# Optimization experiments

Measured on AMD Instinct MI355X. Metric: run time of the kernel, lower is better.

## Reference

```python
import jax, jax.numpy as jnp
import numpy as np

B, N, E = 16, 10000, 160000
C_IN, C_SP, C_OUT = 32, 16, 32


def _glorot(key, shape):
    s = float(np.sqrt(6.0 / (shape[0] + shape[1])))
    return jax.random.uniform(key, shape, jnp.float32, -s, s)


def setup_inputs() -> dict:
    key = jax.random.key(0)
    ks = jax.random.split(key, 12)
    X = jax.random.normal(ks[0], (B, N, C_IN), jnp.float32)
    edge_index1 = jax.random.randint(ks[1], (2, E), 0, N)
    edge_weight1 = jax.random.uniform(ks[2], (E,), jnp.float32)
    res_n_id1 = jnp.arange(N)
    edge_index2 = jax.random.randint(ks[3], (2, E), 0, N)
    edge_weight2 = jax.random.uniform(ks[4], (E,), jnp.float32)
    res_n_id2 = jnp.arange(N)
    # conv1 params (in=C_IN, out=C_SP, edge_channels=1, concat=True)
    amp_w1 = _glorot(ks[5], (1, C_IN))            # [edge_ch, in]
    gate_w1 = _glorot(ks[6], (2 * C_IN + 1, 1))   # Linear(2*in+edge_ch, 1)
    gate_b1 = jnp.zeros((1,), jnp.float32)
    w1 = _glorot(ks[7], (2 * C_IN, C_SP))         # concat weight
    b1 = jnp.zeros((C_SP,), jnp.float32)
    # conv2 params (in=C_SP, out=C_OUT)
    amp_w2 = _glorot(ks[8], (1, C_SP))
    gate_w2 = _glorot(ks[9], (2 * C_SP + 1, 1))
    gate_b2 = jnp.zeros((1,), jnp.float32)
    w2 = _glorot(ks[10], (2 * C_SP, C_OUT))
    b2 = jnp.zeros((C_OUT,), jnp.float32)
    return dict(X=X, edge_index1=edge_index1, edge_weight1=edge_weight1, res_n_id1=res_n_id1,
                edge_index2=edge_index2, edge_weight2=edge_weight2, res_n_id2=res_n_id2,
                amp_w1=amp_w1, gate_w1=gate_w1, gate_b1=gate_b1, w1=w1, b1=b1,
                amp_w2=amp_w2, gate_w2=gate_w2, gate_b2=gate_b2, w2=w2, b2=b2)


def _sagela(x_src, x_dst, edge_index, edge_weight, amp_w, gate_w, gate_b, w, b):
    # x_src: [B, N_src, C], x_dst: [B, N_dst, C]
    src, dst = edge_index[0], edge_index[1]
    n_dst = x_dst.shape[1]
    C = x_src.shape[-1]
    x_j = x_src[:, src]                       # [B, E, C] gathered source feats
    x_i = x_dst[:, dst]                       # [B, E, C] gathered target feats
    e = edge_weight[:, None]                  # [E, 1] edge features
    # gate_linear(cat[x_i, x_j, e]) split into three matmuls (same math)
    wg_i, wg_j, wg_e = gate_w[:C], gate_w[C:2 * C], gate_w[2 * C:]
    lamb = jax.nn.sigmoid(x_i @ wg_i + x_j @ wg_j + (e @ wg_e)[None] + gate_b)  # [B, E, 1]
    amp = e @ amp_w                           # [E, C] edge amplification
    msg = amp[None, :, :] * x_j * lamb        # [B, E, C]
    # mean aggregation over incoming edges (scatter-add / count)
    aggr = jnp.zeros((x_src.shape[0], n_dst, C), msg.dtype).at[:, dst].add(msg)
    cnt = jnp.zeros((n_dst,), msg.dtype).at[dst].add(1.0)
    aggr = aggr / jnp.maximum(cnt, 1.0)[None, :, None]
    out = jnp.concatenate([x_dst, aggr], axis=-1) @ w + b  # [B, N_dst, out]
    return out


def reference(X, edge_index1, edge_weight1, res_n_id1, edge_index2, edge_weight2, res_n_id2,
              amp_w1, gate_w1, gate_b1, w1, b1, amp_w2, gate_w2, gate_b2, w2, b2):
    h = _sagela(X, X[:, res_n_id1], edge_index1, edge_weight1, amp_w1, gate_w1, gate_b1, w1, b1)
    h = jax.nn.leaky_relu(h, 0.01)
    out = _sagela(h, h[:, res_n_id2], edge_index2, edge_weight2, amp_w2, gate_w2, gate_b2, w2, b2)
    return out
```

## Files before the change

kernel.cpp:

```cpp
#include <hip/hip_runtime.h>
#include <math.h>

#define B 16
#define N 10000
#define E 160000
#define CAP 96

__device__ __forceinline__ ushort f2bf(float v) {
    uint u = __float_as_uint(v);
    u = (u + 0x7fffu + ((u >> 16) & 1u)) >> 16;
    return (ushort)u;
}
__device__ __forceinline__ float bf2f(ushort u) { return __uint_as_float(((uint)u) << 16); }
__device__ __forceinline__ float bf2f_lo(uint u) { return __uint_as_float(u << 16); }
__device__ __forceinline__ float bf2f_hi(uint u) { return __uint_as_float(u & 0xffff0000u); }
__device__ __forceinline__ float dec_ew(uint u) {
    return ((float)(u >> 14) + 0.5f) * (1.0f / 262144.0f);
}

__global__ __launch_bounds__(256)
void prep_bucket_kernel(const float* __restrict__ X,
                        const float* __restrict__ gate_w1,
                        const int* __restrict__ ei1, const float* __restrict__ ew1,
                        const int* __restrict__ ei2, const float* __restrict__ ew2,
                        ushort* __restrict__ xt,
                        float* __restrict__ gi, float* __restrict__ gj,
                        int* __restrict__ bcount1, uint* __restrict__ bucket1,
                        int* __restrict__ bcount2, uint* __restrict__ bucket2) {
    int gtid = blockIdx.x * 256 + threadIdx.x;
    int gs = gridDim.x * 256;

    for (int t = gtid; t < 2 * E; t += gs) {
        if (t < E) {
            int d = ei1[E + t];
            int pos = atomicAdd(&bcount1[d], 1);
            if (pos < CAP) {
                uint q = (uint)(ew1[t] * 262144.0f);
                if (q > 262143u) q = 262143u;
                bucket1[d * CAP + pos] = (q << 14) | (uint)ei1[t];
            }
        } else {
            int e = t - E;
            int d = ei2[E + e];
            int pos = atomicAdd(&bcount2[d], 1);
            if (pos < CAP) {
                uint q = (uint)(ew2[e] * 262144.0f);
                if (q > 262143u) q = 262143u;
                bucket2[d * CAP + pos] = (q << 14) | (uint)ei2[e];
            }
        }
    }
    for (int t = gtid; t < N * B * 32; t += gs) {
        int c = t & 31;
        int r = t >> 5;
        int b = r & 15;
        int n = r >> 4;
        float v = X[((size_t)b * N + n) * 32 + c];
        xt[t] = f2bf(v);
        float pi = v * gate_w1[c];
        float pj = v * gate_w1[32 + c];
        #pragma unroll
        for (int off = 16; off; off >>= 1) {
            pi += __shfl_xor(pi, off, 32);
            pj += __shfl_xor(pj, off, 32);
        }
        if (c == 0) { gi[r] = pi; gj[r] = pj; }
    }
}

__global__ __launch_bounds__(256, 8)
void agg_dense1_kernel(const float* __restrict__ X,
                       const uint2* __restrict__ xt2,
                       const float* __restrict__ gi,
                       const float* __restrict__ gj,
                       const int* __restrict__ bcount,
                       const uint* __restrict__ bucket,
                       const float* __restrict__ gate_w,
                       const float* __restrict__ gate_b,
                       const float* __restrict__ amp_w,
                       const float* __restrict__ w1,
                       const float* __restrict__ b1,
                       const float* __restrict__ gate_w2,
                       ushort* __restrict__ htb,
                       float* __restrict__ gi2, float* __restrict__ gj2) {
    __shared__ uint  s_eb[CAP];
    __shared__ float s_coef[CAP * 16];
    __shared__ float s_gi[16];
    __shared__ __align__(16) float s_x[16][36];
    __shared__ __align__(16) float s_feat[16][36];
    __shared__ __align__(16) float s_wmT[16 * 68];

    int n = blockIdx.x;
    int tid = threadIdx.x;

    int cnt = bcount[n];
    int deg = cnt < CAP ? cnt : CAP;
    if (tid < deg) s_eb[tid] = bucket[n * CAP + tid];
    for (int i = tid; i < 1024; i += 256) s_wmT[(i & 15) * 68 + (i >> 4)] = w1[i];
    for (int i = tid; i < 512; i += 256) {
        int b = i >> 5, c = i & 31;
        s_x[b][c] = X[((size_t)b * N + n) * 32 + c];
    }
    if (tid < 16) s_gi[tid] = gi[n * 16 + tid] + gate_b[0];
    __syncthreads();

    float wge = gate_w[64];
    for (int p = tid; p < deg * 16; p += 256) {
        int k = p >> 4, b = p & 15;
        uint pr = s_eb[k];
        float w = dec_ew(pr);
        float z = s_gi[b] + gj[(pr & 0x3FFFu) * 16 + b] + w * wge;
        s_coef[p] = w / (1.0f + __expf(-z));
    }
    __syncthreads();

    int wv = tid >> 6, l = tid & 63;
    int h = l >> 5;
    int b = 4 * wv + ((l & 31) >> 3);
    int c4 = l & 7;
    uint boff = (uint)b * 8 + c4;
    float a0 = 0.f, a1 = 0.f, a2 = 0.f, a3 = 0.f;
    int k = 0;
    for (; k + 7 < deg; k += 8) {
        uint p0 = s_eb[k + h],     p1 = s_eb[k + 2 + h];
        uint p2 = s_eb[k + 4 + h], p3 = s_eb[k + 6 + h];
        float c0 = s_coef[((k + h) << 4) | b],     c1 = s_coef[((k + 2 + h) << 4) | b];
        float c2 = s_coef[((k + 4 + h) << 4) | b], c3 = s_coef[((k + 6 + h) << 4) | b];
        uint2 u0 = xt2[(p0 & 0x3FFFu) * 128 + boff];
        uint2 u1 = xt2[(p1 & 0x3FFFu) * 128 + boff];
        uint2 u2 = xt2[(p2 & 0x3FFFu) * 128 + boff];
        uint2 u3 = xt2[(p3 & 0x3FFFu) * 128 + boff];
        a0 += c0 * bf2f_lo(u0.x) + c1 * bf2f_lo(u1.x) + c2 * bf2f_lo(u2.x) + c3 * bf2f_lo(u3.x);
        a1 += c0 * bf2f_hi(u0.x) + c1 * bf2f_hi(u1.x) + c2 * bf2f_hi(u2.x) + c3 * bf2f_hi(u3.x);
        a2 += c0 * bf2f_lo(u0.y) + c1 * bf2f_lo(u1.y) + c2 * bf2f_lo(u2.y) + c3 * bf2f_lo(u3.y);
        a3 += c0 * bf2f_hi(u0.y) + c1 * bf2f_hi(u1.y) + c2 * bf2f_hi(u2.y) + c3 * bf2f_hi(u3.y);
    }
    for (; k < deg; k += 2) {
        int kk = k + h;
        bool v = kk < deg;
        uint pr = s_eb[v ? kk : 0];
        float cc = v ? s_coef[(kk << 4) | b] : 0.f;
        uint2 u = xt2[(pr & 0x3FFFu) * 128 + boff];
        a0 += cc * bf2f_lo(u.x); a1 += cc * bf2f_hi(u.x);
        a2 += cc * bf2f_lo(u.y); a3 += cc * bf2f_hi(u.y);
    }
    a0 += __shfl_xor(a0, 32, 64);
    a1 += __shfl_xor(a1, 32, 64);
    a2 += __shfl_xor(a2, 32, 64);
    a3 += __shfl_xor(a3, 32, 64);
    if (h == 0) {
        float inv = 1.0f / fmaxf((float)cnt, 1.0f);
        s_feat[b][4 * c4]     = a0 * amp_w[4 * c4] * inv;
        s_feat[b][4 * c4 + 1] = a1 * amp_w[4 * c4 + 1] * inv;
        s_feat[b][4 * c4 + 2] = a2 * amp_w[4 * c4 + 2] * inv;
        s_feat[b][4 * c4 + 3] = a3 * amp_w[4 * c4 + 3] * inv;
    }
    __syncthreads();

    {
        int o = tid & 15, bb = tid >> 4;
        const float4* wr4 = (const float4*)&s_wmT[o * 68];
        const float4* x4  = (const float4*)&s_x[bb][0];
        const float4* f4  = (const float4*)&s_feat[bb][0];
        float d = b1[o];
        #pragma unroll
        for (int q = 0; q < 8; ++q) {
            float4 wv = wr4[q],     xv = x4[q];
            float4 wf = wr4[8 + q], fv = f4[q];
            d += xv.x * wv.x + xv.y * wv.y + xv.z * wv.z + xv.w * wv.w;
            d += fv.x * wf.x + fv.y * wf.y + fv.z * wf.z + fv.w * wf.w;
        }
        d = d > 0.0f ? d : 0.01f * d;
        htb[((size_t)n * 16 + bb) * 16 + o] = f2bf(d);
        float pi = d * gate_w2[o];
        float pj = d * gate_w2[16 + o];
        #pragma unroll
        for (int off = 8; off; off >>= 1) {
            pi += __shfl_xor(pi, off, 16);
            pj += __shfl_xor(pj, off, 16);
        }
        if (o == 0) { gi2[n * 16 + bb] = pi; gj2[n * 16 + bb] = pj; }
    }
}

__global__ __launch_bounds__(256, 8)
void agg_dense2_kernel(const ushort* __restrict__ htb,
                       const uint2* __restrict__ htb2,
                       const float* __restrict__ gi,
                       const float* __restrict__ gj,
                       const int* __restrict__ bcount,
                       const uint* __restrict__ bucket,
                       const float* __restrict__ gate_w,
                       const float* __restrict__ gate_b,
                       const float* __restrict__ amp_w,
                       const float* __restrict__ w2,
                       const float* __restrict__ b2,
                       float* __restrict__ out) {
    __shared__ uint  s_eb[CAP];
    __shared__ float s_coef[CAP * 16];
    __shared__ float s_gi[16];
    __shared__ __align__(16) float s_x[16][20];
    __shared__ __align__(16) float s_feat[16][20];
    __shared__ __align__(16) float s_wmT[32 * 36];

    int n = blockIdx.x;
    int tid = threadIdx.x;

    int cnt = bcount[n];
    int deg = cnt < CAP ? cnt : CAP;
    if (tid < deg) s_eb[tid] = bucket[n * CAP + tid];
    for (int i = tid; i < 1024; i += 256) s_wmT[(i & 31) * 36 + (i >> 5)] = w2[i];
    {
        int b = tid >> 4, c = tid & 15;
        s_x[b][c] = bf2f(htb[(size_t)n * 256 + b * 16 + c]);
    }
    if (tid < 16) s_gi[tid] = gi[n * 16 + tid] + gate_b[0];
    __syncthreads();

    float wge = gate_w[32];
    for (int p = tid; p < deg * 16; p += 256) {
        int k = p >> 4, b = p & 15;
        uint pr = s_eb[k];
        float w = dec_ew(pr);
        float z = s_gi[b] + gj[(pr & 0x3FFFu) * 16 + b] + w * wge;
        s_coef[p] = w / (1.0f + __expf(-z));
    }
    __syncthreads();

    int wv = tid >> 6, l = tid & 63;
    int qd = l >> 4;
    int b = 4 * wv + ((l & 15) >> 2);
    int c4 = l & 3;
    uint boff = (uint)b * 4 + c4;
    float a0 = 0.f, a1 = 0.f, a2 = 0.f, a3 = 0.f;
    int k = 0;
    for (; k + 7 < deg; k += 8) {
        uint p0 = s_eb[k + qd], p1 = s_eb[k + 4 + qd];
        float c0 = s_coef[((k + qd) << 4) | b];
        float c1 = s_coef[((k + 4 + qd) << 4) | b];
        uint2 u0 = htb2[(p0 & 0x3FFFu) * 64 + boff];
        uint2 u1 = htb2[(p1 & 0x3FFFu) * 64 + boff];
        a0 += c0 * bf2f_lo(u0.x) + c1 * bf2f_lo(u1.x);
        a1 += c0 * bf2f_hi(u0.x) + c1 * bf2f_hi(u1.x);
        a2 += c0 * bf2f_lo(u0.y) + c1 * bf2f_lo(u1.y);
        a3 += c0 * bf2f_hi(u0.y) + c1 * bf2f_hi(u1.y);
    }
    for (; k < deg; k += 4) {
        int kk = k + qd;
        bool v = kk < deg;
        uint pr = s_eb[v ? kk : 0];
        float cc = v ? s_coef[(kk << 4) | b] : 0.f;
        uint2 u = htb2[(pr & 0x3FFFu) * 64 + boff];
        a0 += cc * bf2f_lo(u.x); a1 += cc * bf2f_hi(u.x);
        a2 += cc * bf2f_lo(u.y); a3 += cc * bf2f_hi(u.y);
    }
    a0 += __shfl_xor(a0, 16, 64); a0 += __shfl_xor(a0, 32, 64);
    a1 += __shfl_xor(a1, 16, 64); a1 += __shfl_xor(a1, 32, 64);
    a2 += __shfl_xor(a2, 16, 64); a2 += __shfl_xor(a2, 32, 64);
    a3 += __shfl_xor(a3, 16, 64); a3 += __shfl_xor(a3, 32, 64);
    if (qd == 0) {
        float inv = 1.0f / fmaxf((float)cnt, 1.0f);
        s_feat[b][4 * c4]     = a0 * amp_w[4 * c4] * inv;
        s_feat[b][4 * c4 + 1] = a1 * amp_w[4 * c4 + 1] * inv;
        s_feat[b][4 * c4 + 2] = a2 * amp_w[4 * c4 + 2] * inv;
        s_feat[b][4 * c4 + 3] = a3 * amp_w[4 * c4 + 3] * inv;
    }
    __syncthreads();

    int o = tid & 15, bb = tid >> 4;
    const float4* wr0 = (const float4*)&s_wmT[o * 36];
    const float4* wr1 = (const float4*)&s_wmT[(o + 16) * 36];
    const float4* x4  = (const float4*)&s_x[bb][0];
    const float4* f4  = (const float4*)&s_feat[bb][0];
    float d0 = b2[o], d1 = b2[o + 16];
    #pragma unroll
    for (int q = 0; q < 4; ++q) {
        float4 xv = x4[q], fv = f4[q];
        float4 w0a = wr0[q], w0b = wr0[4 + q];
        float4 w1a = wr1[q], w1b = wr1[4 + q];
        d0 += xv.x * w0a.x + xv.y * w0a.y + xv.z * w0a.z + xv.w * w0a.w;
        d0 += fv.x * w0b.x + fv.y * w0b.y + fv.z * w0b.z + fv.w * w0b.w;
        d1 += xv.x * w1a.x + xv.y * w1a.y + xv.z * w1a.z + xv.w * w1a.w;
        d1 += fv.x * w1b.x + fv.y * w1b.y + fv.z * w1b.z + fv.w * w1b.w;
    }
    size_t ob = ((size_t)bb * N + n) * 32;
    out[ob + o] = d0;
    out[ob + o + 16] = d1;
}

extern "C" void kernel_launch(void* const* d_in, const int* in_sizes, int n_in,
                              void* d_out, int out_size, void* d_ws, size_t ws_size,
                              hipStream_t stream) {
    const float* X       = (const float*)d_in[0];
    const int*   ei1     = (const int*)  d_in[1];
    const float* ew1     = (const float*)d_in[2];
    const int*   ei2     = (const int*)  d_in[4];
    const float* ew2     = (const float*)d_in[5];
    const float* amp_w1  = (const float*)d_in[7];
    const float* gate_w1 = (const float*)d_in[8];
    const float* gate_b1 = (const float*)d_in[9];
    const float* w1      = (const float*)d_in[10];
    const float* b1      = (const float*)d_in[11];
    const float* amp_w2  = (const float*)d_in[12];
    const float* gate_w2 = (const float*)d_in[13];
    const float* gate_b2 = (const float*)d_in[14];
    const float* w2      = (const float*)d_in[15];
    const float* b2      = (const float*)d_in[16];
    float* out = (float*)d_out;

    char* p = (char*)d_ws;
    ushort* xt     = (ushort*)p; p += (size_t)N * B * 32 * sizeof(ushort);
    ushort* htb    = (ushort*)p; p += (size_t)N * B * 16 * sizeof(ushort);
    float* gi1     = (float*)p;  p += (size_t)N * B * sizeof(float);
    float* gj1     = (float*)p;  p += (size_t)N * B * sizeof(float);
    float* gi2     = (float*)p;  p += (size_t)N * B * sizeof(float);
    float* gj2     = (float*)p;  p += (size_t)N * B * sizeof(float);
    uint*  bucket1 = (uint*)p;   p += (size_t)N * CAP * sizeof(uint);
    uint*  bucket2 = (uint*)p;   p += (size_t)N * CAP * sizeof(uint);
    int*   bcount1 = (int*)p;    p += (size_t)N * sizeof(int);
    int*   bcount2 = (int*)p;    p += (size_t)N * sizeof(int);

    hipMemsetAsync(bcount1, 0, 2 * (size_t)N * sizeof(int), stream);
    prep_bucket_kernel<<<2048, 256, 0, stream>>>(
        X, gate_w1, ei1, ew1, ei2, ew2, xt, gi1, gj1,
        bcount1, bucket1, bcount2, bucket2);

    agg_dense1_kernel<<<N, 256, 0, stream>>>(
        X, (const uint2*)xt, gi1, gj1, bcount1, bucket1,
        gate_w1, gate_b1, amp_w1, w1, b1, gate_w2, htb, gi2, gj2);

    agg_dense2_kernel<<<N, 256, 0, stream>>>(
        htb, (const uint2*)htb, gi2, gj2, bcount2, bucket2,
        gate_w2, gate_b2, amp_w2, w2, b2, out);
}
```

Measured before the change: 203.6 us.

## Split per-node aggregation blocks across batch groups with smaller thread blocks

Each aggregation kernel now launches one 128-thread block per (node, batch-group) pair instead of one 256-thread block per node. Layer 1 splits the batch into 4 groups of 4 and layer 2 into 2 groups of 8, with the shared-memory buffers and thread mappings resized to match. The goal is more, smaller blocks for better load balance across degree-skewed nodes and lower shared-memory use per block. The cost is that each block reloads the weight matrix and the edge bucket, so that redundant work grows with the number of groups, and each gathered row segment is narrower.

```diff
diff --git a/kernel.cpp b/kernel.cpp
--- a/kernel.cpp
+++ b/kernel.cpp
@@ -68,7 +68,7 @@
     }
 }
 
-__global__ __launch_bounds__(256, 8)
+__global__ __launch_bounds__(128, 8)
 void agg_dense1_kernel(const float* __restrict__ X,
                        const uint2* __restrict__ xt2,
                        const float* __restrict__ gi,
@@ -84,94 +84,91 @@
                        ushort* __restrict__ htb,
                        float* __restrict__ gi2, float* __restrict__ gj2) {
     __shared__ uint  s_eb[CAP];
-    __shared__ float s_coef[CAP * 16];
-    __shared__ float s_gi[16];
-    __shared__ __align__(16) float s_x[16][36];
-    __shared__ __align__(16) float s_feat[16][36];
+    __shared__ float s_coef[CAP * 4];
+    __shared__ float s_gi[4];
+    __shared__ __align__(16) float s_x[4][36];
+    __shared__ __align__(16) float s_feat[4][36];
     __shared__ __align__(16) float s_wmT[16 * 68];
 
-    int n = blockIdx.x;
+    int bid = blockIdx.x;
+    int bg = bid / N;
+    int n = bid - bg * N;
     int tid = threadIdx.x;
 
     int cnt = bcount[n];
     int deg = cnt < CAP ? cnt : CAP;
     if (tid < deg) s_eb[tid] = bucket[n * CAP + tid];
-    for (int i = tid; i < 1024; i += 256) s_wmT[(i & 15) * 68 + (i >> 4)] = w1[i];
-    for (int i = tid; i < 512; i += 256) {
-        int b = i >> 5, c = i & 31;
-        s_x[b][c] = X[((size_t)b * N + n) * 32 + c];
-    }
-    if (tid < 16) s_gi[tid] = gi[n * 16 + tid] + gate_b[0];
+    for (int i = tid; i < 1024; i += 128) s_wmT[(i & 15) * 68 + (i >> 4)] = w1[i];
+    {
+        int bl = tid >> 5, c = tid & 31;
+        s_x[bl][c] = X[((size_t)(bg * 4 + bl) * N + n) * 32 + c];
+    }
+    if (tid < 4) s_gi[tid] = gi[n * 16 + bg * 4 + tid] + gate_b[0];
     __syncthreads();
 
     float wge = gate_w[64];
-    for (int p = tid; p < deg * 16; p += 256) {
-        int k = p >> 4, b = p & 15;
+    for (int p = tid; p < deg * 4; p += 128) {
+        int k = p >> 2, bl = p & 3;
         uint pr = s_eb[k];
         float w = dec_ew(pr);
-        float z = s_gi[b] + gj[(pr & 0x3FFFu) * 16 + b] + w * wge;
+        float z = s_gi[bl] + gj[(pr & 0x3FFFu) * 16 + bg * 4 + bl] + w * wge;
         s_coef[p] = w / (1.0f + __expf(-z));
     }
     __syncthreads();
 
     int wv = tid >> 6, l = tid & 63;
-    int h = l >> 5;
-    int b = 4 * wv + ((l & 31) >> 3);
     int c4 = l & 7;
-    uint boff = (uint)b * 8 + c4;
+    int bl = 2 * wv + ((l >> 3) & 1);
+    int h = l >> 4;
+    uint boff = (uint)(bg * 4 + bl) * 8 + c4;
     float a0 = 0.f, a1 = 0.f, a2 = 0.f, a3 = 0.f;
-    int k = 0;
-    for (; k + 7 < deg; k += 8) {
-        uint p0 = s_eb[k + h],     p1 = s_eb[k + 2 + h];
-        uint p2 = s_eb[k + 4 + h], p3 = s_eb[k + 6 + h];
-        float c0 = s_coef[((k + h) << 4) | b],     c1 = s_coef[((k + 2 + h) << 4) | b];
-        float c2 = s_coef[((k + 4 + h) << 4) | b], c3 = s_coef[((k + 6 + h) << 4) | b];
-        uint2 u0 = xt2[(p0 & 0x3FFFu) * 128 + boff];
-        uint2 u1 = xt2[(p1 & 0x3FFFu) * 128 + boff];
-        uint2 u2 = xt2[(p2 & 0x3FFFu) * 128 + boff];
-        uint2 u3 = xt2[(p3 & 0x3FFFu) * 128 + boff];
-        a0 += c0 * bf2f_lo(u0.x) + c1 * bf2f_lo(u1.x) + c2 * bf2f_lo(u2.x) + c3 * bf2f_lo(u3.x);
-        a1 += c0 * bf2f_hi(u0.x) + c1 * bf2f_hi(u1.x) + c2 * bf2f_hi(u2.x) + c3 * bf2f_hi(u3.x);
-        a2 += c0 * bf2f_lo(u0.y) + c1 * bf2f_lo(u1.y) + c2 * bf2f_lo(u2.y) + c3 * bf2f_lo(u3.y);
-        a3 += c0 * bf2f_hi(u0.y) + c1 * bf2f_hi(u1.y) + c2 * bf2f_hi(u2.y) + c3 * bf2f_hi(u3.y);
-    }
-    for (; k < deg; k += 2) {
-        int kk = k + h;
-        bool v = kk < deg;
-        uint pr = s_eb[v ? kk : 0];
-        float cc = v ? s_coef[(kk << 4) | b] : 0.f;
-        uint2 u = xt2[(pr & 0x3FFFu) * 128 + boff];
+    int k = h;
+    for (; k + 4 < deg; k += 8) {
+        uint p0 = s_eb[k], p1 = s_eb[k + 4];
+        float c0 = s_coef[k * 4 + bl], c1 = s_coef[(k + 4) * 4 + bl];
+        uint2 u0 = xt2[(p0 & 0x3FFFu) * 128u + boff];
+        uint2 u1 = xt2[(p1 & 0x3FFFu) * 128u + boff];
+        a0 += c0 * bf2f_lo(u0.x) + c1 * bf2f_lo(u1.x);
+        a1 += c0 * bf2f_hi(u0.x) + c1 * bf2f_hi(u1.x);
+        a2 += c0 * bf2f_lo(u0.y) + c1 * bf2f_lo(u1.y);
+        a3 += c0 * bf2f_hi(u0.y) + c1 * bf2f_hi(u1.y);
+    }
+    if (k < deg) {
+        uint pr = s_eb[k];
+        float cc = s_coef[k * 4 + bl];
+        uint2 u = xt2[(pr & 0x3FFFu) * 128u + boff];
         a0 += cc * bf2f_lo(u.x); a1 += cc * bf2f_hi(u.x);
         a2 += cc * bf2f_lo(u.y); a3 += cc * bf2f_hi(u.y);
     }
-    a0 += __shfl_xor(a0, 32, 64);
-    a1 += __shfl_xor(a1, 32, 64);
-    a2 += __shfl_xor(a2, 32, 64);
-    a3 += __shfl_xor(a3, 32, 64);
+    a0 += __shfl_xor(a0, 16, 64); a0 += __shfl_xor(a0, 32, 64);
+    a1 += __shfl_xor(a1, 16, 64); a1 += __shfl_xor(a1, 32, 64);
+    a2 += __shfl_xor(a2, 16, 64); a2 += __shfl_xor(a2, 32, 64);
+    a3 += __shfl_xor(a3, 16, 64); a3 += __shfl_xor(a3, 32, 64);
     if (h == 0) {
         float inv = 1.0f / fmaxf((float)cnt, 1.0f);
-        s_feat[b][4 * c4]     = a0 * amp_w[4 * c4] * inv;
-        s_feat[b][4 * c4 + 1] = a1 * amp_w[4 * c4 + 1] * inv;
-        s_feat[b][4 * c4 + 2] = a2 * amp_w[4 * c4 + 2] * inv;
-        s_feat[b][4 * c4 + 3] = a3 * amp_w[4 * c4 + 3] * inv;
-    }
-    __syncthreads();
-
-    {
-        int o = tid & 15, bb = tid >> 4;
+        s_feat[bl][4 * c4]     = a0 * amp_w[4 * c4] * inv;
+        s_feat[bl][4 * c4 + 1] = a1 * amp_w[4 * c4 + 1] * inv;
+        s_feat[bl][4 * c4 + 2] = a2 * amp_w[4 * c4 + 2] * inv;
+        s_feat[bl][4 * c4 + 3] = a3 * amp_w[4 * c4 + 3] * inv;
+    }
+    __syncthreads();
+
+    if (tid < 64) {
+        int o = tid & 15, b_l = tid >> 4;
         const float4* wr4 = (const float4*)&s_wmT[o * 68];
-        const float4* x4  = (const float4*)&s_x[bb][0];
-        const float4* f4  = (const float4*)&s_feat[bb][0];
+        const float4* x4  = (const float4*)&s_x[b_l][0];
+        const float4* f4  = (const float4*)&s_feat[b_l][0];
         float d = b1[o];
         #pragma unroll
         for (int q = 0; q < 8; ++q) {
-            float4 wv = wr4[q],     xv = x4[q];
+            float4 wvv = wr4[q],    xv = x4[q];
             float4 wf = wr4[8 + q], fv = f4[q];
-            d += xv.x * wv.x + xv.y * wv.y + xv.z * wv.z + xv.w * wv.w;
+            d += xv.x * wvv.x + xv.y * wvv.y + xv.z * wvv.z + xv.w * wvv.w;
             d += fv.x * wf.x + fv.y * wf.y + fv.z * wf.z + fv.w * wf.w;
         }
         d = d > 0.0f ? d : 0.01f * d;
-        htb[((size_t)n * 16 + bb) * 16 + o] = f2bf(d);
+        int b = bg * 4 + b_l;
+        htb[((size_t)n * 16 + b) * 16 + o] = f2bf(d);
         float pi = d * gate_w2[o];
         float pj = d * gate_w2[16 + o];
         #pragma unroll
@@ -179,11 +176,11 @@
             pi += __shfl_xor(pi, off, 16);
             pj += __shfl_xor(pj, off, 16);
         }
-        if (o == 0) { gi2[n * 16 + bb] = pi; gj2[n * 16 + bb] = pj; }
-    }
-}
-
-__global__ __launch_bounds__(256, 8)
+        if (o == 0) { gi2[n * 16 + b] = pi; gj2[n * 16 + b] = pj; }
+    }
+}
+
+__global__ __launch_bounds__(128, 8)
 void agg_dense2_kernel(const ushort* __restrict__ htb,
                        const uint2* __restrict__ htb2,
                        const float* __restrict__ gi,
@@ -197,60 +194,59 @@
                        const float* __restrict__ b2,
                        float* __restrict__ out) {
     __shared__ uint  s_eb[CAP];
-    __shared__ float s_coef[CAP * 16];
-    __shared__ float s_gi[16];
-    __shared__ __align__(16) float s_x[16][20];
-    __shared__ __align__(16) float s_feat[16][20];
+    __shared__ float s_coef[CAP * 8];
+    __shared__ float s_gi[8];
+    __shared__ __align__(16) float s_x[8][20];
+    __shared__ __align__(16) float s_feat[8][20];
     __shared__ __align__(16) float s_wmT[32 * 36];
 
-    int n = blockIdx.x;
+    int bid = blockIdx.x;
+    int bg = bid / N;
+    int n = bid - bg * N;
     int tid = threadIdx.x;
 
     int cnt = bcount[n];
     int deg = cnt < CAP ? cnt : CAP;
     if (tid < deg) s_eb[tid] = bucket[n * CAP + tid];
-    for (int i = tid; i < 1024; i += 256) s_wmT[(i & 31) * 36 + (i >> 5)] = w2[i];
+    for (int i = tid; i < 1024; i += 128) s_wmT[(i & 31) * 36 + (i >> 5)] = w2[i];
     {
-        int b = tid >> 4, c = tid & 15;
-        s_x[b][c] = bf2f(htb[(size_t)n * 256 + b * 16 + c]);
-    }
-    if (tid < 16) s_gi[tid] = gi[n * 16 + tid] + gate_b[0];
+        int bl = tid >> 4, c = tid & 15;
+        s_x[bl][c] = bf2f(htb[(size_t)n * 256 + (bg * 8 + bl) * 16 + c]);
+    }
+    if (tid < 8) s_gi[tid] = gi[n * 16 + bg * 8 + tid] + gate_b[0];
     __syncthreads();
 
     float wge = gate_w[32];
-    for (int p = tid; p < deg * 16; p += 256) {
-        int k = p >> 4, b = p & 15;
+    for (int p = tid; p < deg * 8; p += 128) {
+        int k = p >> 3, bl = p & 7;
         uint pr = s_eb[k];
         float w = dec_ew(pr);
-        float z = s_gi[b] + gj[(pr & 0x3FFFu) * 16 + b] + w * wge;
+        float z = s_gi[bl] + gj[(pr & 0x3FFFu) * 16 + bg * 8 + bl] + w * wge;
         s_coef[p] = w / (1.0f + __expf(-z));
     }
     __syncthreads();
 
     int wv = tid >> 6, l = tid & 63;
-    int qd = l >> 4;
-    int b = 4 * wv + ((l & 15) >> 2);
     int c4 = l & 3;
-    uint boff = (uint)b * 4 + c4;
+    int bl = 4 * wv + ((l >> 2) & 3);
+    int h = l >> 4;
+    uint boff = (uint)(bg * 8 + bl) * 4 + c4;
     float a0 = 0.f, a1 = 0.f, a2 = 0.f, a3 = 0.f;
-    int k = 0;
-    for (; k + 7 < deg; k += 8) {
-        uint p0 = s_eb[k + qd], p1 = s_eb[k + 4 + qd];
-        float c0 = s_coef[((k + qd) << 4) | b];
-        float c1 = s_coef[((k + 4 + qd) << 4) | b];
-        uint2 u0 = htb2[(p0 & 0x3FFFu) * 64 + boff];
-        uint2 u1 = htb2[(p1 & 0x3FFFu) * 64 + boff];
+    int k = h;
+    for (; k + 4 < deg; k += 8) {
+        uint p0 = s_eb[k], p1 = s_eb[k + 4];
+        float c0 = s_coef[k * 8 + bl], c1 = s_coef[(k + 4) * 8 + bl];
+        uint2 u0 = htb2[(p0 & 0x3FFFu) * 64u + boff];
+        uint2 u1 = htb2[(p1 & 0x3FFFu) * 64u + boff];
         a0 += c0 * bf2f_lo(u0.x) + c1 * bf2f_lo(u1.x);
         a1 += c0 * bf2f_hi(u0.x) + c1 * bf2f_hi(u1.x);
         a2 += c0 * bf2f_lo(u0.y) + c1 * bf2f_lo(u1.y);
         a3 += c0 * bf2f_hi(u0.y) + c1 * bf2f_hi(u1.y);
     }
-    for (; k < deg; k += 4) {
-        int kk = k + qd;
-        bool v = kk < deg;
-        uint pr = s_eb[v ? kk : 0];
-        float cc = v ? s_coef[(kk << 4) | b] : 0.f;
-        uint2 u = htb2[(pr & 0x3FFFu) * 64 + boff];
+    if (k < deg) {
+        uint pr = s_eb[k];
+        float cc = s_coef[k * 8 + bl];
+        uint2 u = htb2[(pr & 0x3FFFu) * 64u + boff];
         a0 += cc * bf2f_lo(u.x); a1 += cc * bf2f_hi(u.x);
         a2 += cc * bf2f_lo(u.y); a3 += cc * bf2f_hi(u.y);
     }
@@ -258,34 +254,36 @@
     a1 += __shfl_xor(a1, 16, 64); a1 += __shfl_xor(a1, 32, 64);
     a2 += __shfl_xor(a2, 16, 64); a2 += __shfl_xor(a2, 32, 64);
     a3 += __shfl_xor(a3, 16, 64); a3 += __shfl_xor(a3, 32, 64);
-    if (qd == 0) {
+    if (h == 0) {
         float inv = 1.0f / fmaxf((float)cnt, 1.0f);
-        s_feat[b][4 * c4]     = a0 * amp_w[4 * c4] * inv;
-        s_feat[b][4 * c4 + 1] = a1 * amp_w[4 * c4 + 1] * inv;
-        s_feat[b][4 * c4 + 2] = a2 * amp_w[4 * c4 + 2] * inv;
-        s_feat[b][4 * c4 + 3] = a3 * amp_w[4 * c4 + 3] * inv;
-    }
-    __syncthreads();
-
-    int o = tid & 15, bb = tid >> 4;
-    const float4* wr0 = (const float4*)&s_wmT[o * 36];
-    const float4* wr1 = (const float4*)&s_wmT[(o + 16) * 36];
-    const float4* x4  = (const float4*)&s_x[bb][0];
-    const float4* f4  = (const float4*)&s_feat[bb][0];
-    float d0 = b2[o], d1 = b2[o + 16];
-    #pragma unroll
-    for (int q = 0; q < 4; ++q) {
-        float4 xv = x4[q], fv = f4[q];
-        float4 w0a = wr0[q], w0b = wr0[4 + q];
-        float4 w1a = wr1[q], w1b = wr1[4 + q];
-        d0 += xv.x * w0a.x + xv.y * w0a.y + xv.z * w0a.z + xv.w * w0a.w;
-        d0 += fv.x * w0b.x + fv.y * w0b.y + fv.z * w0b.z + fv.w * w0b.w;
-        d1 += xv.x * w1a.x + xv.y * w1a.y + xv.z * w1a.z + xv.w * w1a.w;
-        d1 += fv.x * w1b.x + fv.y * w1b.y + fv.z * w1b.z + fv.w * w1b.w;
-    }
-    size_t ob = ((size_t)bb * N + n) * 32;
-    out[ob + o] = d0;
-    out[ob + o + 16] = d1;
+        s_feat[bl][4 * c4]     = a0 * amp_w[4 * c4] * inv;
+        s_feat[bl][4 * c4 + 1] = a1 * amp_w[4 * c4 + 1] * inv;
+        s_feat[bl][4 * c4 + 2] = a2 * amp_w[4 * c4 + 2] * inv;
+        s_feat[bl][4 * c4 + 3] = a3 * amp_w[4 * c4 + 3] * inv;
+    }
+    __syncthreads();
+
+    {
+        int o = tid & 15, b_l = tid >> 4;
+        const float4* wr0 = (const float4*)&s_wmT[o * 36];
+        const float4* wr1 = (const float4*)&s_wmT[(o + 16) * 36];
+        const float4* x4  = (const float4*)&s_x[b_l][0];
+        const float4* f4  = (const float4*)&s_feat[b_l][0];
+        float d0 = b2[o], d1 = b2[o + 16];
+        #pragma unroll
+        for (int q = 0; q < 4; ++q) {
+            float4 xv = x4[q], fv = f4[q];
+            float4 w0a = wr0[q], w0b = wr0[4 + q];
+            float4 w1a = wr1[q], w1b = wr1[4 + q];
+            d0 += xv.x * w0a.x + xv.y * w0a.y + xv.z * w0a.z + xv.w * w0a.w;
+            d0 += fv.x * w0b.x + fv.y * w0b.y + fv.z * w0b.z + fv.w * w0b.w;
+            d1 += xv.x * w1a.x + xv.y * w1a.y + xv.z * w1a.z + xv.w * w1a.w;
+            d1 += fv.x * w1b.x + fv.y * w1b.y + fv.z * w1b.z + fv.w * w1b.w;
+        }
+        size_t ob = ((size_t)(bg * 8 + b_l) * N + n) * 32;
+        out[ob + o] = d0;
+        out[ob + o + 16] = d1;
+    }
 }
 
 extern "C" void kernel_launch(void* const* d_in, const int* in_sizes, int n_in,
@@ -325,11 +323,11 @@
         X, gate_w1, ei1, ew1, ei2, ew2, xt, gi1, gj1,
         bcount1, bucket1, bcount2, bucket2);
 
-    agg_dense1_kernel<<<N, 256, 0, stream>>>(
+    agg_dense1_kernel<<<4 * N, 128, 0, stream>>>(
         X, (const uint2*)xt, gi1, gj1, bcount1, bucket1,
         gate_w1, gate_b1, amp_w1, w1, b1, gate_w2, htb, gi2, gj2);
 
-    agg_dense2_kernel<<<N, 256, 0, stream>>>(
+    agg_dense2_kernel<<<2 * N, 128, 0, stream>>>(
         htb, (const uint2*)htb, gi2, gj2, bcount2, bucket2,
         gate_w2, gate_b2, amp_w2, w2, b2, out);
 }
```

Measured after the change: 230.3 us. 13.1% more time.

## Widen gathers to 16-byte loads and pre-transpose weights in prep kernel

Applied to the files above, without the earlier changes.

The per-edge feature gathers in both aggregation kernels now use uint4 loads of 8 bf16 channels instead of uint2 loads. The lane-to-edge mapping and the shuffle reductions are changed to match. The prep kernel now handles one row per thread with float4 reads and packed uint4 bf16 stores, and it writes pre-transposed copies of w1 and w2 so each block loads them with coalesced float4 reads. The intent is fewer, wider memory transactions on the gather-bound path, at the cost of less edge-level parallelism per wave and more reduction shuffles.

```diff
diff --git a/kernel.cpp b/kernel.cpp
--- a/kernel.cpp
+++ b/kernel.cpp
@@ -23,8 +23,11 @@
                         const float* __restrict__ gate_w1,
                         const int* __restrict__ ei1, const float* __restrict__ ew1,
                         const int* __restrict__ ei2, const float* __restrict__ ew2,
+                        const float* __restrict__ w1,
+                        const float* __restrict__ w2,
                         ushort* __restrict__ xt,
                         float* __restrict__ gi, float* __restrict__ gj,
+                        float* __restrict__ w1T, float* __restrict__ w2T,
                         int* __restrict__ bcount1, uint* __restrict__ bucket1,
                         int* __restrict__ bcount2, uint* __restrict__ bucket2) {
     int gtid = blockIdx.x * 256 + threadIdx.x;
@@ -50,27 +53,39 @@
             }
         }
     }
-    for (int t = gtid; t < N * B * 32; t += gs) {
-        int c = t & 31;
-        int r = t >> 5;
-        int b = r & 15;
-        int n = r >> 4;
-        float v = X[((size_t)b * N + n) * 32 + c];
-        xt[t] = f2bf(v);
-        float pi = v * gate_w1[c];
-        float pj = v * gate_w1[32 + c];
+
+    for (int t = gtid; t < N * B; t += gs) {
+        int b = t / N;
+        int n = t - b * N;
+        int r = n * 16 + b;
+        const float4* xr = (const float4*)(X + ((size_t)b * N + n) * 32);
+        float pi = 0.f, pj = 0.f;
+        union { uint u[16]; uint4 v4[4]; } pk;
         #pragma unroll
-        for (int off = 16; off; off >>= 1) {
-            pi += __shfl_xor(pi, off, 32);
-            pj += __shfl_xor(pj, off, 32);
-        }
-        if (c == 0) { gi[r] = pi; gj[r] = pj; }
+        for (int q = 0; q < 8; ++q) {
+            float4 v = xr[q];
+            pi += v.x * gate_w1[4*q]   + v.y * gate_w1[4*q+1]
+                + v.z * gate_w1[4*q+2] + v.w * gate_w1[4*q+3];
+            pj += v.x * gate_w1[32+4*q]   + v.y * gate_w1[32+4*q+1]
+                + v.z * gate_w1[32+4*q+2] + v.w * gate_w1[32+4*q+3];
+            pk.u[2*q]   = (uint)f2bf(v.x) | ((uint)f2bf(v.y) << 16);
+            pk.u[2*q+1] = (uint)f2bf(v.z) | ((uint)f2bf(v.w) << 16);
+        }
+        uint4* dst = (uint4*)(xt + (size_t)r * 32);
+        dst[0] = pk.v4[0]; dst[1] = pk.v4[1];
+        dst[2] = pk.v4[2]; dst[3] = pk.v4[3];
+        gi[r] = pi; gj[r] = pj;
+    }
+
+    if (gtid < 1024) {
+        w1T[(gtid & 15) * 64 + (gtid >> 4)] = w1[gtid];
+        w2T[(gtid & 31) * 32 + (gtid >> 5)] = w2[gtid];
     }
 }
 
 __global__ __launch_bounds__(256, 8)
 void agg_dense1_kernel(const float* __restrict__ X,
-                       const uint2* __restrict__ xt2,
+                       const uint4* __restrict__ xt4,
                        const float* __restrict__ gi,
                        const float* __restrict__ gj,
                        const int* __restrict__ bcount,
@@ -78,7 +93,7 @@
                        const float* __restrict__ gate_w,
                        const float* __restrict__ gate_b,
                        const float* __restrict__ amp_w,
-                       const float* __restrict__ w1,
+                       const float* __restrict__ w1T,
                        const float* __restrict__ b1,
                        const float* __restrict__ gate_w2,
                        ushort* __restrict__ htb,
@@ -95,11 +110,15 @@
 
     int cnt = bcount[n];
     int deg = cnt < CAP ? cnt : CAP;
-    if (tid < deg) s_eb[tid] = bucket[n * CAP + tid];
-    for (int i = tid; i < 1024; i += 256) s_wmT[(i & 15) * 68 + (i >> 4)] = w1[i];
-    for (int i = tid; i < 512; i += 256) {
-        int b = i >> 5, c = i & 31;
-        s_x[b][c] = X[((size_t)b * N + n) * 32 + c];
+    if (tid < CAP / 4)
+        ((uint4*)s_eb)[tid] = ((const uint4*)(bucket + (size_t)n * CAP))[tid];
+    {
+        int o = tid >> 4, k4 = tid & 15;
+        *(float4*)&s_wmT[o * 68 + k4 * 4] = ((const float4*)w1T)[o * 16 + k4];
+    }
+    if (tid < 128) {
+        int b = tid >> 3, q = tid & 7;
+        *(float4*)&s_x[b][q * 4] = ((const float4*)(X + ((size_t)b * N + n) * 32))[q];
     }
     if (tid < 16) s_gi[tid] = gi[n * 16 + tid] + gate_b[0];
     __syncthreads();
@@ -115,45 +134,55 @@
     __syncthreads();
 
     int wv = tid >> 6, l = tid & 63;
-    int h = l >> 5;
-    int b = 4 * wv + ((l & 31) >> 3);
-    int c4 = l & 7;
-    uint boff = (uint)b * 8 + c4;
+    int c8 = l & 3;
+    int b  = 4 * wv + ((l >> 2) & 3);
+    int h  = l >> 4;
+    uint boff = (uint)b * 4 + c8;
     float a0 = 0.f, a1 = 0.f, a2 = 0.f, a3 = 0.f;
-    int k = 0;
-    for (; k + 7 < deg; k += 8) {
-        uint p0 = s_eb[k + h],     p1 = s_eb[k + 2 + h];
-        uint p2 = s_eb[k + 4 + h], p3 = s_eb[k + 6 + h];
-        float c0 = s_coef[((k + h) << 4) | b],     c1 = s_coef[((k + 2 + h) << 4) | b];
-        float c2 = s_coef[((k + 4 + h) << 4) | b], c3 = s_coef[((k + 6 + h) << 4) | b];
-        uint2 u0 = xt2[(p0 & 0x3FFFu) * 128 + boff];
-        uint2 u1 = xt2[(p1 & 0x3FFFu) * 128 + boff];
-        uint2 u2 = xt2[(p2 & 0x3FFFu) * 128 + boff];
-        uint2 u3 = xt2[(p3 & 0x3FFFu) * 128 + boff];
-        a0 += c0 * bf2f_lo(u0.x) + c1 * bf2f_lo(u1.x) + c2 * bf2f_lo(u2.x) + c3 * bf2f_lo(u3.x);
-        a1 += c0 * bf2f_hi(u0.x) + c1 * bf2f_hi(u1.x) + c2 * bf2f_hi(u2.x) + c3 * bf2f_hi(u3.x);
-        a2 += c0 * bf2f_lo(u0.y) + c1 * bf2f_lo(u1.y) + c2 * bf2f_lo(u2.y) + c3 * bf2f_lo(u3.y);
-        a3 += c0 * bf2f_hi(u0.y) + c1 * bf2f_hi(u1.y) + c2 * bf2f_hi(u2.y) + c3 * bf2f_hi(u3.y);
-    }
-    for (; k < deg; k += 2) {
-        int kk = k + h;
-        bool v = kk < deg;
-        uint pr = s_eb[v ? kk : 0];
-        float cc = v ? s_coef[(kk << 4) | b] : 0.f;
-        uint2 u = xt2[(pr & 0x3FFFu) * 128 + boff];
+    float a4 = 0.f, a5 = 0.f, a6 = 0.f, a7 = 0.f;
+    int k = h;
+    for (; k + 4 < deg; k += 8) {
+        uint p0 = s_eb[k], p1 = s_eb[k + 4];
+        float c0 = s_coef[(k << 4) | b], c1 = s_coef[((k + 4) << 4) | b];
+        uint4 u0 = xt4[(p0 & 0x3FFFu) * 64u + boff];
+        uint4 u1 = xt4[(p1 & 0x3FFFu) * 64u + boff];
+        a0 += c0 * bf2f_lo(u0.x) + c1 * bf2f_lo(u1.x);
+        a1 += c0 * bf2f_hi(u0.x) + c1 * bf2f_hi(u1.x);
+        a2 += c0 * bf2f_lo(u0.y) + c1 * bf2f_lo(u1.y);
+        a3 += c0 * bf2f_hi(u0.y) + c1 * bf2f_hi(u1.y);
+        a4 += c0 * bf2f_lo(u0.z) + c1 * bf2f_lo(u1.z);
+        a5 += c0 * bf2f_hi(u0.z) + c1 * bf2f_hi(u1.z);
+        a6 += c0 * bf2f_lo(u0.w) + c1 * bf2f_lo(u1.w);
+        a7 += c0 * bf2f_hi(u0.w) + c1 * bf2f_hi(u1.w);
+    }
+    if (k < deg) {
+        uint pr = s_eb[k];
+        float cc = s_coef[(k << 4) | b];
+        uint4 u = xt4[(pr & 0x3FFFu) * 64u + boff];
         a0 += cc * bf2f_lo(u.x); a1 += cc * bf2f_hi(u.x);
         a2 += cc * bf2f_lo(u.y); a3 += cc * bf2f_hi(u.y);
-    }
-    a0 += __shfl_xor(a0, 32, 64);
-    a1 += __shfl_xor(a1, 32, 64);
-    a2 += __shfl_xor(a2, 32, 64);
-    a3 += __shfl_xor(a3, 32, 64);
+        a4 += cc * bf2f_lo(u.z); a5 += cc * bf2f_hi(u.z);
+        a6 += cc * bf2f_lo(u.w); a7 += cc * bf2f_hi(u.w);
+    }
+    a0 += __shfl_xor(a0, 16, 64); a0 += __shfl_xor(a0, 32, 64);
+    a1 += __shfl_xor(a1, 16, 64); a1 += __shfl_xor(a1, 32, 64);
+    a2 += __shfl_xor(a2, 16, 64); a2 += __shfl_xor(a2, 32, 64);
+    a3 += __shfl_xor(a3, 16, 64); a3 += __shfl_xor(a3, 32, 64);
+    a4 += __shfl_xor(a4, 16, 64); a4 += __shfl_xor(a4, 32, 64);
+    a5 += __shfl_xor(a5, 16, 64); a5 += __shfl_xor(a5, 32, 64);
+    a6 += __shfl_xor(a6, 16, 64); a6 += __shfl_xor(a6, 32, 64);
+    a7 += __shfl_xor(a7, 16, 64); a7 += __shfl_xor(a7, 32, 64);
     if (h == 0) {
         float inv = 1.0f / fmaxf((float)cnt, 1.0f);
-        s_feat[b][4 * c4]     = a0 * amp_w[4 * c4] * inv;
-        s_feat[b][4 * c4 + 1] = a1 * amp_w[4 * c4 + 1] * inv;
-        s_feat[b][4 * c4 + 2] = a2 * amp_w[4 * c4 + 2] * inv;
-        s_feat[b][4 * c4 + 3] = a3 * amp_w[4 * c4 + 3] * inv;
+        int cb = 8 * c8;
+        s_feat[b][cb]     = a0 * amp_w[cb]     * inv;
+        s_feat[b][cb + 1] = a1 * amp_w[cb + 1] * inv;
+        s_feat[b][cb + 2] = a2 * amp_w[cb + 2] * inv;
+        s_feat[b][cb + 3] = a3 * amp_w[cb + 3] * inv;
+        s_feat[b][cb + 4] = a4 * amp_w[cb + 4] * inv;
+        s_feat[b][cb + 5] = a5 * amp_w[cb + 5] * inv;
+        s_feat[b][cb + 6] = a6 * amp_w[cb + 6] * inv;
+        s_feat[b][cb + 7] = a7 * amp_w[cb + 7] * inv;
     }
     __syncthreads();
 
@@ -165,9 +194,9 @@
         float d = b1[o];
         #pragma unroll
         for (int q = 0; q < 8; ++q) {
-            float4 wv = wr4[q],     xv = x4[q];
+            float4 wvv = wr4[q],    xv = x4[q];
             float4 wf = wr4[8 + q], fv = f4[q];
-            d += xv.x * wv.x + xv.y * wv.y + xv.z * wv.z + xv.w * wv.w;
+            d += xv.x * wvv.x + xv.y * wvv.y + xv.z * wvv.z + xv.w * wvv.w;
             d += fv.x * wf.x + fv.y * wf.y + fv.z * wf.z + fv.w * wf.w;
         }
         d = d > 0.0f ? d : 0.01f * d;
@@ -184,8 +213,7 @@
 }
 
 __global__ __launch_bounds__(256, 8)
-void agg_dense2_kernel(const ushort* __restrict__ htb,
-                       const uint2* __restrict__ htb2,
+void agg_dense2_kernel(const uint4* __restrict__ htb4,
                        const float* __restrict__ gi,
                        const float* __restrict__ gj,
                        const int* __restrict__ bcount,
@@ -193,7 +221,7 @@
                        const float* __restrict__ gate_w,
                        const float* __restrict__ gate_b,
                        const float* __restrict__ amp_w,
-                       const float* __restrict__ w2,
+                       const float* __restrict__ w2T,
                        const float* __restrict__ b2,
                        float* __restrict__ out) {
     __shared__ uint  s_eb[CAP];
@@ -208,11 +236,22 @@
 
     int cnt = bcount[n];
     int deg = cnt < CAP ? cnt : CAP;
-    if (tid < deg) s_eb[tid] = bucket[n * CAP + tid];
-    for (int i = tid; i < 1024; i += 256) s_wmT[(i & 31) * 36 + (i >> 5)] = w2[i];
+    if (tid < CAP / 4)
+        ((uint4*)s_eb)[tid] = ((const uint4*)(bucket + (size_t)n * CAP))[tid];
     {
-        int b = tid >> 4, c = tid & 15;
-        s_x[b][c] = bf2f(htb[(size_t)n * 256 + b * 16 + c]);
+        int o = tid >> 3, k4 = tid & 7;
+        *(float4*)&s_wmT[o * 36 + k4 * 4] = ((const float4*)w2T)[o * 8 + k4];
+    }
+    if (tid < 32) {
+        uint4 u = htb4[(size_t)n * 32 + tid];
+        int b = tid >> 1, cb = (tid & 1) * 8;
+        float4 f0, f1;
+        f0.x = bf2f_lo(u.x); f0.y = bf2f_hi(u.x);
+        f0.z = bf2f_lo(u.y); f0.w = bf2f_hi(u.y);
+        f1.x = bf2f_lo(u.z); f1.y = bf2f_hi(u.z);
+        f1.z = bf2f_lo(u.w); f1.w = bf2f_hi(u.w);
+        *(float4*)&s_x[b][cb]     = f0;
+        *(float4*)&s_x[b][cb + 4] = f1;
     }
     if (tid < 16) s_gi[tid] = gi[n * 16 + tid] + gate_b[0];
     __syncthreads();
@@ -228,64 +267,79 @@
     __syncthreads();
 
     int wv = tid >> 6, l = tid & 63;
-    int qd = l >> 4;
-    int b = 4 * wv + ((l & 15) >> 2);
-    int c4 = l & 3;
-    uint boff = (uint)b * 4 + c4;
+    int c8 = l & 1;
+    int b  = 4 * wv + ((l >> 1) & 3);
+    int qd = l >> 3;
+    uint boff = (uint)b * 2 + c8;
     float a0 = 0.f, a1 = 0.f, a2 = 0.f, a3 = 0.f;
-    int k = 0;
-    for (; k + 7 < deg; k += 8) {
-        uint p0 = s_eb[k + qd], p1 = s_eb[k + 4 + qd];
-        float c0 = s_coef[((k + qd) << 4) | b];
-        float c1 = s_coef[((k + 4 + qd) << 4) | b];
-        uint2 u0 = htb2[(p0 & 0x3FFFu) * 64 + boff];
-        uint2 u1 = htb2[(p1 & 0x3FFFu) * 64 + boff];
+    float a4 = 0.f, a5 = 0.f, a6 = 0.f, a7 = 0.f;
+    int k = qd;
+    for (; k + 8 < deg; k += 16) {
+        uint p0 = s_eb[k], p1 = s_eb[k + 8];
+        float c0 = s_coef[(k << 4) | b], c1 = s_coef[((k + 8) << 4) | b];
+        uint4 u0 = htb4[(p0 & 0x3FFFu) * 32u + boff];
+        uint4 u1 = htb4[(p1 & 0x3FFFu) * 32u + boff];
         a0 += c0 * bf2f_lo(u0.x) + c1 * bf2f_lo(u1.x);
         a1 += c0 * bf2f_hi(u0.x) + c1 * bf2f_hi(u1.x);
         a2 += c0 * bf2f_lo(u0.y) + c1 * bf2f_lo(u1.y);
         a3 += c0 * bf2f_hi(u0.y) + c1 * bf2f_hi(u1.y);
-    }
-    for (; k < deg; k += 4) {
-        int kk = k + qd;
-        bool v = kk < deg;
-        uint pr = s_eb[v ? kk : 0];
-        float cc = v ? s_coef[(kk << 4) | b] : 0.f;
-        uint2 u = htb2[(pr & 0x3FFFu) * 64 + boff];
+        a4 += c0 * bf2f_lo(u0.z) + c1 * bf2f_lo(u1.z);
+        a5 += c0 * bf2f_hi(u0.z) + c1 * bf2f_hi(u1.z);
+        a6 += c0 * bf2f_lo(u0.w) + c1 * bf2f_lo(u1.w);
+        a7 += c0 * bf2f_hi(u0.w) + c1 * bf2f_hi(u1.w);
+    }
+    if (k < deg) {
+        uint pr = s_eb[k];
+        float cc = s_coef[(k << 4) | b];
+        uint4 u = htb4[(pr & 0x3FFFu) * 32u + boff];
         a0 += cc * bf2f_lo(u.x); a1 += cc * bf2f_hi(u.x);
         a2 += cc * bf2f_lo(u.y); a3 += cc * bf2f_hi(u.y);
-    }
-    a0 += __shfl_xor(a0, 16, 64); a0 += __shfl_xor(a0, 32, 64);
-    a1 += __shfl_xor(a1, 16, 64); a1 += __shfl_xor(a1, 32, 64);
-    a2 += __shfl_xor(a2, 16, 64); a2 += __shfl_xor(a2, 32, 64);
-    a3 += __shfl_xor(a3, 16, 64); a3 += __shfl_xor(a3, 32, 64);
+        a4 += cc * bf2f_lo(u.z); a5 += cc * bf2f_hi(u.z);
+        a6 += cc * bf2f_lo(u.w); a7 += cc * bf2f_hi(u.w);
+    }
+    a0 += __shfl_xor(a0, 8, 64); a0 += __shfl_xor(a0, 16, 64); a0 += __shfl_xor(a0, 32, 64);
+    a1 += __shfl_xor(a1, 8, 64); a1 += __shfl_xor(a1, 16, 64); a1 += __shfl_xor(a1, 32, 64);
+    a2 += __shfl_xor(a2, 8, 64); a2 += __shfl_xor(a2, 16, 64); a2 += __shfl_xor(a2, 32, 64);
+    a3 += __shfl_xor(a3, 8, 64); a3 += __shfl_xor(a3, 16, 64); a3 += __shfl_xor(a3, 32, 64);
+    a4 += __shfl_xor(a4, 8, 64); a4 += __shfl_xor(a4, 16, 64); a4 += __shfl_xor(a4, 32, 64);
+    a5 += __shfl_xor(a5, 8, 64); a5 += __shfl_xor(a5, 16, 64); a5 += __shfl_xor(a5, 32, 64);
+    a6 += __shfl_xor(a6, 8, 64); a6 += __shfl_xor(a6, 16, 64); a6 += __shfl_xor(a6, 32, 64);
+    a7 += __shfl_xor(a7, 8, 64); a7 += __shfl_xor(a7, 16, 64); a7 += __shfl_xor(a7, 32, 64);
     if (qd == 0) {
         float inv = 1.0f / fmaxf((float)cnt, 1.0f);
-        s_feat[b][4 * c4]     = a0 * amp_w[4 * c4] * inv;
-        s_feat[b][4 * c4 + 1] = a1 * amp_w[4 * c4 + 1] * inv;
-        s_feat[b][4 * c4 + 2] = a2 * amp_w[4 * c4 + 2] * inv;
-        s_feat[b][4 * c4 + 3] = a3 * amp_w[4 * c4 + 3] * inv;
-    }
-    __syncthreads();
-
-    int o = tid & 15, bb = tid >> 4;
-    const float4* wr0 = (const float4*)&s_wmT[o * 36];
-    const float4* wr1 = (const float4*)&s_wmT[(o + 16) * 36];
-    const float4* x4  = (const float4*)&s_x[bb][0];
-    const float4* f4  = (const float4*)&s_feat[bb][0];
-    float d0 = b2[o], d1 = b2[o + 16];
-    #pragma unroll
-    for (int q = 0; q < 4; ++q) {
-        float4 xv = x4[q], fv = f4[q];
-        float4 w0a = wr0[q], w0b = wr0[4 + q];
-        float4 w1a = wr1[q], w1b = wr1[4 + q];
-        d0 += xv.x * w0a.x + xv.y * w0a.y + xv.z * w0a.z + xv.w * w0a.w;
-        d0 += fv.x * w0b.x + fv.y * w0b.y + fv.z * w0b.z + fv.w * w0b.w;
-        d1 += xv.x * w1a.x + xv.y * w1a.y + xv.z * w1a.z + xv.w * w1a.w;
-        d1 += fv.x * w1b.x + fv.y * w1b.y + fv.z * w1b.z + fv.w * w1b.w;
-    }
-    size_t ob = ((size_t)bb * N + n) * 32;
-    out[ob + o] = d0;
-    out[ob + o + 16] = d1;
+        int cb = 8 * c8;
+        s_feat[b][cb]     = a0 * amp_w[cb]     * inv;
+        s_feat[b][cb + 1] = a1 * amp_w[cb + 1] * inv;
+        s_feat[b][cb + 2] = a2 * amp_w[cb + 2] * inv;
+        s_feat[b][cb + 3] = a3 * amp_w[cb + 3] * inv;
+        s_feat[b][cb + 4] = a4 * amp_w[cb + 4] * inv;
+        s_feat[b][cb + 5] = a5 * amp_w[cb + 5] * inv;
+        s_feat[b][cb + 6] = a6 * amp_w[cb + 6] * inv;
+        s_feat[b][cb + 7] = a7 * amp_w[cb + 7] * inv;
+    }
+    __syncthreads();
+
+    {
+        int o2 = tid & 15, bb = tid >> 4;
+        const float4* wr0 = (const float4*)&s_wmT[(2 * o2) * 36];
+        const float4* wr1 = (const float4*)&s_wmT[(2 * o2 + 1) * 36];
+        const float4* x4  = (const float4*)&s_x[bb][0];
+        const float4* f4  = (const float4*)&s_feat[bb][0];
+        float d0 = b2[2 * o2], d1 = b2[2 * o2 + 1];
+        #pragma unroll
+        for (int q = 0; q < 4; ++q) {
+            float4 xv = x4[q], fv = f4[q];
+            float4 w0a = wr0[q], w0b = wr0[4 + q];
+            float4 w1a = wr1[q], w1b = wr1[4 + q];
+            d0 += xv.x * w0a.x + xv.y * w0a.y + xv.z * w0a.z + xv.w * w0a.w;
+            d0 += fv.x * w0b.x + fv.y * w0b.y + fv.z * w0b.z + fv.w * w0b.w;
+            d1 += xv.x * w1a.x + xv.y * w1a.y + xv.z * w1a.z + xv.w * w1a.w;
+            d1 += fv.x * w1b.x + fv.y * w1b.y + fv.z * w1b.z + fv.w * w1b.w;
+        }
+        size_t ob = ((size_t)bb * N + n) * 32;
+        float2 r; r.x = d0; r.y = d1;
+        *(float2*)(out + ob + 2 * o2) = r;
+    }
 }
 
 extern "C" void kernel_launch(void* const* d_in, const int* in_sizes, int n_in,
@@ -319,17 +373,19 @@
     uint*  bucket2 = (uint*)p;   p += (size_t)N * CAP * sizeof(uint);
     int*   bcount1 = (int*)p;    p += (size_t)N * sizeof(int);
     int*   bcount2 = (int*)p;    p += (size_t)N * sizeof(int);
+    float* w1T     = (float*)p;  p += 1024 * sizeof(float);
+    float* w2T     = (float*)p;  p += 1024 * sizeof(float);
 
     hipMemsetAsync(bcount1, 0, 2 * (size_t)N * sizeof(int), stream);
     prep_bucket_kernel<<<2048, 256, 0, stream>>>(
-        X, gate_w1, ei1, ew1, ei2, ew2, xt, gi1, gj1,
+        X, gate_w1, ei1, ew1, ei2, ew2, w1, w2, xt, gi1, gj1, w1T, w2T,
         bcount1, bucket1, bcount2, bucket2);
 
     agg_dense1_kernel<<<N, 256, 0, stream>>>(
-        X, (const uint2*)xt, gi1, gj1, bcount1, bucket1,
-        gate_w1, gate_b1, amp_w1, w1, b1, gate_w2, htb, gi2, gj2);
+        X, (const uint4*)xt, gi1, gj1, bcount1, bucket1,
+        gate_w1, gate_b1, amp_w1, w1T, b1, gate_w2, htb, gi2, gj2);
 
     agg_dense2_kernel<<<N, 256, 0, stream>>>(
-        htb, (const uint2*)htb, gi2, gj2, bcount2, bucket2,
-        gate_w2, gate_b2, amp_w2, w2, b2, out);
-}
+        (const uint4*)htb, gi2, gj2, bcount2, bucket2,
+        gate_w2, gate_b2, amp_w2, w2T, b2, out);
+}
```

Result: no change. 199.9 us (-1.8%).
